# Kernel tuning notes

Measured on AMD Instinct MI355X. Metric: run time of the kernel, lower is better.

Reference implementation:

```python
import jax, jax.numpy as jnp
import numpy as np

S, B, IN, OUT = 16, 32, 1024, 1024


def setup_inputs() -> dict:
    key = jax.random.key(0)
    ks = jax.random.split(key, 7)
    return {
        "input": jax.random.normal(ks[0], (S, B, IN), dtype=jnp.float32),
        "w_mu": jax.random.normal(ks[1], (OUT, IN), dtype=jnp.float32) * 0.1 - 3.0,
        "w_std_eta": jax.random.uniform(ks[2], (OUT, IN), dtype=jnp.float32, minval=-4.0, maxval=-2.0),
        "b_mu": jax.random.normal(ks[3], (OUT,), dtype=jnp.float32) * 0.03,
        "b_std_eta": jax.random.uniform(ks[4], (OUT,), dtype=jnp.float32, minval=-0.03, maxval=0.03),
        "eps_w": jax.random.normal(ks[5], (B, OUT, IN), dtype=jnp.float32),
        "eps_b": jax.random.normal(ks[6], (B, OUT), dtype=jnp.float32),
    }


def _kl_to_std_normal(mu, std):
    # KL( N(mu, std) || N(0, 1) ) elementwise, summed
    return jnp.sum(-jnp.log(std) + 0.5 * (std * std + mu * mu) - 0.5)


def reference(input, w_mu, w_std_eta, b_mu, b_std_eta, eps_w, eps_b):
    std_w = 1e-06 + jax.nn.softplus(w_std_eta)          # [OUT, IN]
    std_b = 1e-06 + jax.nn.softplus(b_std_eta)          # [OUT]
    # per-batch-element reparameterized positive weights: [B, OUT, IN]
    w = jnp.exp(w_mu[None, :, :] + std_w[None, :, :] * eps_w)
    b = b_mu[None, :] + std_b[None, :] * eps_b          # [B, OUT]
    # batched linear: for each b-index i: input[:, i, :] @ w[i].T + b[i]
    out = jnp.einsum('sbi,boi->sbo', input, w) + b[None, :, :]  # [S, B, OUT]
    kl_w = _kl_to_std_normal(w_mu, std_w)
    kl_b = _kl_to_std_normal(b_mu, std_b)
    return (out, kl_w, kl_b)
```

## Files before the change

### kernel.cpp

```cpp
#include <hip/hip_runtime.h>


constexpr int S_ = 16, B_ = 32, IN_ = 1024, OUT_ = 1024;

typedef __bf16 bf16x8 __attribute__((ext_vector_type(8)));
typedef float  f32x4  __attribute__((ext_vector_type(4)));

__device__ __forceinline__ float softplus_f(float x) {
    float e = __expf(-fabsf(x));
    return fmaxf(x, 0.0f) + __logf(1.0f + e);
}

__device__ __forceinline__ unsigned bf16_hi(float x) {
    return (__float_as_uint(x) + 0x8000u) & 0xffff0000u;
}

__global__ __launch_bounds__(256) void bpl_pre2(
    const float* __restrict__ input,
    const float* __restrict__ w_mu, const float* __restrict__ w_eta,
    unsigned* __restrict__ tbl,
    __bf16* __restrict__ a_ws,
    float* __restrict__ klw_part)
{
    const int tid = threadIdx.x;

    if (blockIdx.x >= 1024) {
        const int b = blockIdx.x - 1024;
        #pragma unroll
        for (int j = 0; j < 8; ++j) {
            const int c  = tid + j * 256;
            const int k0 = ((c >> 6) << 5) | (((c >> 4) & 3) << 3);
            const int s  = c & 15;
            const float* src = input + ((size_t)s * B_ + b) * IN_ + k0;
            const float4 x0 = *reinterpret_cast<const float4*>(src);
            const float4 x1 = *reinterpret_cast<const float4*>(src + 4);
            bf16x8 v;
            v[0] = (__bf16)x0.x; v[1] = (__bf16)x0.y; v[2] = (__bf16)x0.z; v[3] = (__bf16)x0.w;
            v[4] = (__bf16)x1.x; v[5] = (__bf16)x1.y; v[6] = (__bf16)x1.z; v[7] = (__bf16)x1.w;
            *reinterpret_cast<bf16x8*>(&a_ws[(size_t)b * 16384 + (size_t)c * 8]) = v;
        }
        return;
    }

    __shared__ float red[4];
    const int wid  = tid >> 6;
    const int lane = tid & 63;

    const size_t base = (size_t)blockIdx.x * IN_ + tid * 4;
    const float4 mu = *reinterpret_cast<const float4*>(&w_mu[base]);
    const float4 et = *reinterpret_cast<const float4*>(&w_eta[base]);
    const float m[4] = {mu.x, mu.y, mu.z, mu.w};
    const float e[4] = {et.x, et.y, et.z, et.w};

    uint4 pk;
    unsigned* pku = &pk.x;
    float local = 0.0f;
    #pragma unroll
    for (int j = 0; j < 4; ++j) {
        const float sp  = __logf(1.0f + __expf(e[j])) + 1e-6f;
        const float spl = sp * 1.44269504f;
        const float emu = __expf(m[j]);
        pku[j] = bf16_hi(emu) | (bf16_hi(spl) >> 16);
        local += -__logf(sp) + 0.5f * fmaf(sp, sp, m[j] * m[j]) - 0.5f;
    }
    *reinterpret_cast<uint4*>(&tbl[base]) = pk;

    #pragma unroll
    for (int off = 32; off > 0; off >>= 1) local += __shfl_xor(local, off, 64);
    if (lane == 0) red[wid] = local;
    __syncthreads();
    if (tid == 0) klw_part[blockIdx.x] = red[0] + red[1] + red[2] + red[3];
}

__global__ __launch_bounds__(256, 4) void bpl_fused(
    const unsigned* __restrict__ tbl,
    const __bf16* __restrict__ a_ws,
    const float* __restrict__ eps_w,
    const float* __restrict__ b_mu,
    const float* __restrict__ b_eta,
    const float* __restrict__ eps_b,
    const float* __restrict__ klw_part,
    float* __restrict__ out,
    float* __restrict__ kl)
{
    const int blk = blockIdx.x;
    const int tid = threadIdx.x;

    if (blk == 2048) {
        __shared__ float kred[8];
        const int wid  = tid >> 6;
        const int lane = tid & 63;
        float lw = klw_part[tid] + klw_part[tid + 256]
                 + klw_part[tid + 512] + klw_part[tid + 768];
        float lb = 0.0f;
        #pragma unroll
        for (int h = 0; h < 4; ++h) {
            const int o = tid + h * 256;
            const float sd = softplus_f(b_eta[o]) + 1e-6f;
            const float mm = b_mu[o];
            lb += -__logf(sd) + 0.5f * fmaf(sd, sd, mm * mm) - 0.5f;
        }
        #pragma unroll
        for (int off = 32; off > 0; off >>= 1) {
            lw += __shfl_xor(lw, off, 64);
            lb += __shfl_xor(lb, off, 64);
        }
        if (lane == 0) { kred[wid] = lw; kred[4 + wid] = lb; }
        __syncthreads();
        if (tid == 0) {
            kl[0] = kred[0] + kred[1] + kred[2] + kred[3];
            kl[1] = kred[4] + kred[5] + kred[6] + kred[7];
        }
        return;
    }

    __shared__ __align__(16) float red[4 * 64 * 4];

    const int xcd = blk & 7;
    const int r_  = blk >> 3;
    const int b   = r_ & 31;
    const int ot  = r_ >> 5;
    const int o_base = xcd * 128 + ot * 16;

    const int kq   = tid >> 6;
    const int lane = tid & 63;
    const int on   = lane & 15;
    const int kg0  = lane >> 4;
    const int o_row = o_base + on;

    const int kbase = kq * 256 + kg0 * 8;
    const unsigned* __restrict__ tp = tbl + (size_t)o_row * IN_ + kbase;
    const float* __restrict__ ep = eps_w + ((size_t)b * OUT_ + o_row) * IN_ + kbase;
    const __bf16* __restrict__ ap = a_ws + (size_t)b * 16384 + (size_t)kq * 4096 + lane * 8;

    f32x4 acc = {0.0f, 0.0f, 0.0f, 0.0f};

    uint4  tb0[4], tb1[4];
    float4 ev0[4], ev1[4];
    bf16x8 av[4];

#define BPL_LD(T) do {                                                                    \
        ev0[(T) & 3] = *reinterpret_cast<const float4*>(ep + (T) * 32);                   \
        ev1[(T) & 3] = *reinterpret_cast<const float4*>(ep + (T) * 32 + 4);               \
        tb0[(T) & 3] = *reinterpret_cast<const uint4*>(tp + (T) * 32);                    \
        tb1[(T) & 3] = *reinterpret_cast<const uint4*>(tp + (T) * 32 + 4);                \
        av[(T) & 3]  = *reinterpret_cast<const bf16x8*>(ap + (T) * 512); } while (0)

    BPL_LD(0); BPL_LD(1); BPL_LD(2); BPL_LD(3);

    #pragma unroll
    for (int t = 0; t < 8; ++t) {
        const uint4  u0 = tb0[t & 3], u1 = tb1[t & 3];
        const float4 e0 = ev0[t & 3], e1 = ev1[t & 3];
        const bf16x8 af = av[t & 3];

        const unsigned uu[8] = {u0.x, u0.y, u0.z, u0.w, u1.x, u1.y, u1.z, u1.w};
        const float    ee[8] = {e0.x, e0.y, e0.z, e0.w, e1.x, e1.y, e1.z, e1.w};

        bf16x8 bfrag;
        #pragma unroll
        for (int q = 0; q < 8; ++q) {
            const float emu = __uint_as_float(uu[q] & 0xffff0000u);
            const float spl = __uint_as_float(uu[q] << 16);
            bfrag[q] = (__bf16)(emu * exp2f(spl * ee[q]));
        }

        if (t < 4) BPL_LD(t + 4);

        acc = __builtin_amdgcn_mfma_f32_16x16x32_bf16(af, bfrag, acc, 0, 0, 0);
    }
#undef BPL_LD

    *reinterpret_cast<f32x4*>(&red[(kq * 64 + lane) * 4]) = acc;
    __syncthreads();

    {
        const int s  = tid >> 4;
        const int ol = tid & 15;
        const int srcLane = ((s >> 2) << 4) | ol;
        const int rr = s & 3;
        float v = red[(0 * 64 + srcLane) * 4 + rr] + red[(1 * 64 + srcLane) * 4 + rr]
                + red[(2 * 64 + srcLane) * 4 + rr] + red[(3 * 64 + srcLane) * 4 + rr];
        const int oo = o_base + ol;
        const float bias = fmaf(softplus_f(b_eta[oo]) + 1e-6f,
                                eps_b[(size_t)b * OUT_ + oo], b_mu[oo]);
        out[((size_t)s * B_ + b) * OUT_ + oo] = v + bias;
    }
}

__global__ __launch_bounds__(256) void bpl_pre_fb(
    const float* __restrict__ w_mu, const float* __restrict__ w_eta,
    const float* __restrict__ b_mu, const float* __restrict__ b_eta,
    float* __restrict__ kl)
{
    __shared__ float red[4];
    const int tid  = threadIdx.x;
    const int wid  = tid >> 6;
    const int lane = tid & 63;

    const size_t base = (size_t)blockIdx.x * IN_ + tid * 4;
    const float4 mu = *reinterpret_cast<const float4*>(&w_mu[base]);
    const float4 et = *reinterpret_cast<const float4*>(&w_eta[base]);
    const float m[4] = {mu.x, mu.y, mu.z, mu.w};
    const float e[4] = {et.x, et.y, et.z, et.w};

    float local = 0.0f;
    #pragma unroll
    for (int j = 0; j < 4; ++j) {
        const float sp = __logf(1.0f + __expf(e[j])) + 1e-6f;
        local += -__logf(sp) + 0.5f * fmaf(sp, sp, m[j] * m[j]) - 0.5f;
    }
    #pragma unroll
    for (int off = 32; off > 0; off >>= 1) local += __shfl_xor(local, off, 64);
    if (lane == 0) red[wid] = local;
    __syncthreads();
    if (tid == 0) atomicAdd(&kl[0], red[0] + red[1] + red[2] + red[3]);

    if (blockIdx.x != 0) return;
    float lb = 0.0f;
    #pragma unroll
    for (int j = 0; j < 4; ++j) {
        const int idx = tid * 4 + j;
        const float sd = softplus_f(b_eta[idx]) + 1e-6f;
        const float mm = b_mu[idx];
        lb += -__logf(sd) + 0.5f * fmaf(sd, sd, mm * mm) - 0.5f;
    }
    #pragma unroll
    for (int off = 32; off > 0; off >>= 1) lb += __shfl_xor(lb, off, 64);
    __syncthreads();
    if (lane == 0) red[wid] = lb;
    __syncthreads();
    if (tid == 0) atomicAdd(&kl[1], red[0] + red[1] + red[2] + red[3]);
}

__global__ __launch_bounds__(256, 4) void bpl_mfma_fb(
    const float* __restrict__ input, const float* __restrict__ w_mu,
    const float* __restrict__ w_eta, const float* __restrict__ b_mu,
    const float* __restrict__ b_eta, const float* __restrict__ eps_w,
    const float* __restrict__ eps_b, float* __restrict__ out)
{
    __shared__ __align__(16) __bf16 alds[16384];

    const int blk = blockIdx.x;
    const int xcd = blk & 7;
    const int r_  = blk >> 3;
    const int b   = r_ & 31;
    const int oh  = r_ >> 5;
    const int o_base = (xcd * 2 + oh) * 64;

    const int tid  = threadIdx.x;
    const int wid  = tid >> 6;
    const int lane = tid & 63;

    #pragma unroll
    for (int j = 0; j < 8; ++j) {
        const int c   = tid + j * 256;
        const int s   = c & 15;
        const int kgg = ((c >> 6) << 2) | ((c >> 4) & 3);
        const float* src = input + ((size_t)s * B_ + b) * IN_ + kgg * 8;
        const float4 x0 = *reinterpret_cast<const float4*>(src);
        const float4 x1 = *reinterpret_cast<const float4*>(src + 4);
        bf16x8 v;
        v[0] = (__bf16)x0.x; v[1] = (__bf16)x0.y; v[2] = (__bf16)x0.z; v[3] = (__bf16)x0.w;
        v[4] = (__bf16)x1.x; v[5] = (__bf16)x1.y; v[6] = (__bf16)x1.z; v[7] = (__bf16)x1.w;
        *reinterpret_cast<bf16x8*>(&alds[c * 8]) = v;
    }
    __syncthreads();

    const int on    = lane & 15;
    const int kg0   = lane >> 4;
    const int o_row = o_base + wid * 16 + on;

    const float* __restrict__ mu_p = w_mu  + (size_t)o_row * IN_ + kg0 * 8;
    const float* __restrict__ et_p = w_eta + (size_t)o_row * IN_ + kg0 * 8;
    const float* __restrict__ ep_p = eps_w + ((size_t)b * OUT_ + o_row) * IN_ + kg0 * 8;
    const __bf16* __restrict__ a_p = alds + lane * 8;

    f32x4 acc = {0.0f, 0.0f, 0.0f, 0.0f};
    #pragma unroll
    for (int kt = 0; kt < 32; ++kt) {
        const int i_ = kt * 32;
        const float4 m0 = *reinterpret_cast<const float4*>(mu_p + i_);
        const float4 m1 = *reinterpret_cast<const float4*>(mu_p + i_ + 4);
        const float4 s0 = *reinterpret_cast<const float4*>(et_p + i_);
        const float4 s1 = *reinterpret_cast<const float4*>(et_p + i_ + 4);
        const float4 e0 = *reinterpret_cast<const float4*>(ep_p + i_);
        const float4 e1 = *reinterpret_cast<const float4*>(ep_p + i_ + 4);
        const float mm[8] = {m0.x, m0.y, m0.z, m0.w, m1.x, m1.y, m1.z, m1.w};
        const float ss[8] = {s0.x, s0.y, s0.z, s0.w, s1.x, s1.y, s1.z, s1.w};
        const float ee[8] = {e0.x, e0.y, e0.z, e0.w, e1.x, e1.y, e1.z, e1.w};
        bf16x8 bfrag;
        #pragma unroll
        for (int q = 0; q < 8; ++q) {
            const float sp_ = __logf(1.0f + __expf(ss[q])) + 1e-6f;
            bfrag[q] = (__bf16)__expf(fmaf(sp_, ee[q], mm[q]));
        }
        const bf16x8 afrag = *reinterpret_cast<const bf16x8*>(a_p + kt * 512);
        acc = __builtin_amdgcn_mfma_f32_16x16x32_bf16(afrag, bfrag, acc, 0, 0, 0);
    }

    const float bias = fmaf(softplus_f(b_eta[o_row]) + 1e-6f,
                            eps_b[(size_t)b * OUT_ + o_row], b_mu[o_row]);
    #pragma unroll
    for (int rr = 0; rr < 4; ++rr) {
        const int s = kg0 * 4 + rr;
        out[((size_t)s * B_ + b) * OUT_ + o_row] = acc[rr] + bias;
    }
}

extern "C" void kernel_launch(void* const* d_in, const int* in_sizes, int n_in,
                              void* d_out, int out_size, void* d_ws, size_t ws_size,
                              hipStream_t stream)
{
    const float* input = (const float*)d_in[0];
    const float* w_mu  = (const float*)d_in[1];
    const float* w_eta = (const float*)d_in[2];
    const float* b_mu  = (const float*)d_in[3];
    const float* b_eta = (const float*)d_in[4];
    const float* eps_w = (const float*)d_in[5];
    const float* eps_b = (const float*)d_in[6];

    float* out = (float*)d_out;
    float* kl  = out + (size_t)S_ * B_ * OUT_;

    const size_t TBL_OFF = 0;
    const size_t A_OFF   = (size_t)4 * 1024 * 1024;
    const size_t KLP_OFF = (size_t)5 * 1024 * 1024;
    const size_t NEED    = KLP_OFF + 4096;

    if (ws_size >= NEED) {
        unsigned* tbl  = (unsigned*)((char*)d_ws + TBL_OFF);
        __bf16*   a_ws = (__bf16*)((char*)d_ws + A_OFF);
        float*    klp  = (float*)((char*)d_ws + KLP_OFF);

        bpl_pre2<<<1056, 256, 0, stream>>>(input, w_mu, w_eta, tbl, a_ws, klp);
        bpl_fused<<<2049, 256, 0, stream>>>(tbl, a_ws, eps_w, b_mu, b_eta, eps_b,
                                            klp, out, kl);
    } else {
        hipMemsetAsync(kl, 0, 2 * sizeof(float), stream);
        bpl_pre_fb<<<1024, 256, 0, stream>>>(w_mu, w_eta, b_mu, b_eta, kl);
        bpl_mfma_fb<<<512, 256, 0, stream>>>(input, w_mu, w_eta, b_mu, b_eta,
                                             eps_w, eps_b, out);
    }
}
```

Measured before the change: 43.91 us.

## Stage eps_w through swizzled LDS and pre-permute weight table into fragment order

The fused kernel now uses 512 threads with 8 k-quarters. Each wave loads eps_w rows with fully coalesced float2 reads, stages them in XOR-swizzled shared memory, then reads them back in MFMA fragment order. The precompute kernel writes the packed exp(mu)/softplus table directly in fragment-major layout, so the fused kernel's table loads are contiguous per lane. The goal is to fix strided global access to eps_w and the table, at the cost of 64KB of LDS per block, an extra barrier, and lost software pipelining of loads against compute.

```diff
diff --git a/kernel.cpp b/kernel.cpp
--- a/kernel.cpp
+++ b/kernel.cpp
@@ -18,7 +18,7 @@
 __global__ __launch_bounds__(256) void bpl_pre2(
     const float* __restrict__ input,
     const float* __restrict__ w_mu, const float* __restrict__ w_eta,
-    unsigned* __restrict__ tbl,
+    unsigned* __restrict__ tbl_f,
     __bf16* __restrict__ a_ws,
     float* __restrict__ klw_part)
 {
@@ -45,25 +45,31 @@
     __shared__ float red[4];
     const int wid  = tid >> 6;
     const int lane = tid & 63;
-
-    const size_t base = (size_t)blockIdx.x * IN_ + tid * 4;
+    const int o    = blockIdx.x;
+    const int ot   = o >> 4;
+    const int on   = o & 15;
+
+    const size_t base = (size_t)o * IN_ + tid * 4;
     const float4 mu = *reinterpret_cast<const float4*>(&w_mu[base]);
     const float4 et = *reinterpret_cast<const float4*>(&w_eta[base]);
     const float m[4] = {mu.x, mu.y, mu.z, mu.w};
     const float e[4] = {et.x, et.y, et.z, et.w};
 
-    uint4 pk;
-    unsigned* pku = &pk.x;
     float local = 0.0f;
     #pragma unroll
     for (int j = 0; j < 4; ++j) {
+        const int   i   = tid * 4 + j;
         const float sp  = __logf(1.0f + __expf(e[j])) + 1e-6f;
         const float spl = sp * 1.44269504f;
         const float emu = __expf(m[j]);
-        pku[j] = bf16_hi(emu) | (bf16_hi(spl) >> 16);
+        const unsigned pk = bf16_hi(emu) | (bf16_hi(spl) >> 16);
+        const int kt  = i >> 5;
+        const int kg0 = (i >> 3) & 3;
+        const int jj  = i & 7;
+        const int ln  = kg0 * 16 + on;
+        tbl_f[(((size_t)ot * 32 + kt) * 64 + ln) * 8 + jj] = pk;
         local += -__logf(sp) + 0.5f * fmaf(sp, sp, m[j] * m[j]) - 0.5f;
     }
-    *reinterpret_cast<uint4*>(&tbl[base]) = pk;
 
     #pragma unroll
     for (int off = 32; off > 0; off >>= 1) local += __shfl_xor(local, off, 64);
@@ -72,8 +78,8 @@
     if (tid == 0) klw_part[blockIdx.x] = red[0] + red[1] + red[2] + red[3];
 }
 
-__global__ __launch_bounds__(256, 4) void bpl_fused(
-    const unsigned* __restrict__ tbl,
+__global__ __launch_bounds__(512, 4) void bpl_fused(
+    const unsigned* __restrict__ tbl_f,
     const __bf16* __restrict__ a_ws,
     const float* __restrict__ eps_w,
     const float* __restrict__ b_mu,
@@ -87,75 +93,91 @@
     const int tid = threadIdx.x;
 
     if (blk == 2048) {
-        __shared__ float kred[8];
+        __shared__ float kred[16];
         const int wid  = tid >> 6;
         const int lane = tid & 63;
-        float lw = klw_part[tid] + klw_part[tid + 256]
-                 + klw_part[tid + 512] + klw_part[tid + 768];
+        float lw = klw_part[tid & 1023] * 0.0f;
+        lw = ((tid < 512) ? klw_part[tid] + klw_part[tid + 512] : 0.0f);
         float lb = 0.0f;
-        #pragma unroll
-        for (int h = 0; h < 4; ++h) {
-            const int o = tid + h * 256;
-            const float sd = softplus_f(b_eta[o]) + 1e-6f;
-            const float mm = b_mu[o];
-            lb += -__logf(sd) + 0.5f * fmaf(sd, sd, mm * mm) - 0.5f;
+        {
+            const int o = tid;
+            const float sd0 = softplus_f(b_eta[o]) + 1e-6f;
+            const float m0  = b_mu[o];
+            const float sd1 = softplus_f(b_eta[o + 512]) + 1e-6f;
+            const float m1  = b_mu[o + 512];
+            lb = (-__logf(sd0) + 0.5f * fmaf(sd0, sd0, m0 * m0) - 0.5f)
+               + (-__logf(sd1) + 0.5f * fmaf(sd1, sd1, m1 * m1) - 0.5f);
         }
         #pragma unroll
         for (int off = 32; off > 0; off >>= 1) {
             lw += __shfl_xor(lw, off, 64);
             lb += __shfl_xor(lb, off, 64);
         }
-        if (lane == 0) { kred[wid] = lw; kred[4 + wid] = lb; }
+        if (lane == 0) { kred[wid] = lw; kred[8 + wid] = lb; }
         __syncthreads();
         if (tid == 0) {
-            kl[0] = kred[0] + kred[1] + kred[2] + kred[3];
-            kl[1] = kred[4] + kred[5] + kred[6] + kred[7];
+            float tw = 0.0f, tb = 0.0f;
+            #pragma unroll
+            for (int k = 0; k < 8; ++k) { tw += kred[k]; tb += kred[8 + k]; }
+            kl[0] = tw; kl[1] = tb;
         }
         return;
     }
 
-    __shared__ __align__(16) float red[4 * 64 * 4];
+    __shared__ __align__(16) float smem[16384];
 
     const int xcd = blk & 7;
     const int r_  = blk >> 3;
     const int b   = r_ & 31;
-    const int ot  = r_ >> 5;
-    const int o_base = xcd * 128 + ot * 16;
+    const int otl = r_ >> 5;
+    const int o_base = xcd * 128 + otl * 16;
+    const int ot_g   = o_base >> 4;
 
     const int kq   = tid >> 6;
     const int lane = tid & 63;
     const int on   = lane & 15;
     const int kg0  = lane >> 4;
-    const int o_row = o_base + on;
-
-    const int kbase = kq * 256 + kg0 * 8;
-    const unsigned* __restrict__ tp = tbl + (size_t)o_row * IN_ + kbase;
-    const float* __restrict__ ep = eps_w + ((size_t)b * OUT_ + o_row) * IN_ + kbase;
-    const __bf16* __restrict__ ap = a_ws + (size_t)b * 16384 + (size_t)kq * 4096 + lane * 8;
+
+    const float* eps_base = eps_w + ((size_t)(b * 1024 + o_base)) * 1024 + kq * 128;
+    float2 ev[16];
+    #pragma unroll
+    for (int r = 0; r < 16; ++r)
+        ev[r] = *reinterpret_cast<const float2*>(eps_base + (size_t)r * 1024 + lane * 2);
+
+    const unsigned* tf = tbl_f + (((size_t)ot_g * 32 + kq * 4) * 64 + lane) * 8;
+    uint4 t0[4], t1[4];
+    #pragma unroll
+    for (int t = 0; t < 4; ++t) {
+        t0[t] = *reinterpret_cast<const uint4*>(tf + t * 512);
+        t1[t] = *reinterpret_cast<const uint4*>(tf + t * 512 + 4);
+    }
+
+    const __bf16* ap = a_ws + (size_t)b * 16384 + (size_t)(kq * 4) * 512 + lane * 8;
+    bf16x8 av[4];
+    #pragma unroll
+    for (int t = 0; t < 4; ++t)
+        av[t] = *reinterpret_cast<const bf16x8*>(ap + t * 512);
+
+    char* wbase = (char*)(smem + kq * 2048);
+    #pragma unroll
+    for (int r = 0; r < 16; ++r) {
+        const int byte = (lane * 8) ^ ((r & 7) << 4);
+        *reinterpret_cast<float2*>(wbase + r * 512 + byte) = ev[r];
+    }
+    __syncthreads();
 
     f32x4 acc = {0.0f, 0.0f, 0.0f, 0.0f};
-
-    uint4  tb0[4], tb1[4];
-    float4 ev0[4], ev1[4];
-    bf16x8 av[4];
-
-#define BPL_LD(T) do {                                                                    \
-        ev0[(T) & 3] = *reinterpret_cast<const float4*>(ep + (T) * 32);                   \
-        ev1[(T) & 3] = *reinterpret_cast<const float4*>(ep + (T) * 32 + 4);               \
-        tb0[(T) & 3] = *reinterpret_cast<const uint4*>(tp + (T) * 32);                    \
-        tb1[(T) & 3] = *reinterpret_cast<const uint4*>(tp + (T) * 32 + 4);                \
-        av[(T) & 3]  = *reinterpret_cast<const bf16x8*>(ap + (T) * 512); } while (0)
-
-    BPL_LD(0); BPL_LD(1); BPL_LD(2); BPL_LD(3);
-
-    #pragma unroll
-    for (int t = 0; t < 8; ++t) {
-        const uint4  u0 = tb0[t & 3], u1 = tb1[t & 3];
-        const float4 e0 = ev0[t & 3], e1 = ev1[t & 3];
-        const bf16x8 af = av[t & 3];
-
-        const unsigned uu[8] = {u0.x, u0.y, u0.z, u0.w, u1.x, u1.y, u1.z, u1.w};
-        const float    ee[8] = {e0.x, e0.y, e0.z, e0.w, e1.x, e1.y, e1.z, e1.w};
+    const int sw = (on & 7) << 4;
+    #pragma unroll
+    for (int t = 0; t < 4; ++t) {
+        const f32x4 e0 = *reinterpret_cast<const f32x4*>(
+            wbase + on * 512 + (((t * 128 + kg0 * 32)) ^ sw));
+        const f32x4 e1 = *reinterpret_cast<const f32x4*>(
+            wbase + on * 512 + (((t * 128 + kg0 * 32 + 16)) ^ sw));
+
+        const unsigned uu[8] = {t0[t].x, t0[t].y, t0[t].z, t0[t].w,
+                                t1[t].x, t1[t].y, t1[t].z, t1[t].w};
+        const float    ee[8] = {e0[0], e0[1], e0[2], e0[3], e1[0], e1[1], e1[2], e1[3]};
 
         bf16x8 bfrag;
         #pragma unroll
@@ -164,23 +186,22 @@
             const float spl = __uint_as_float(uu[q] << 16);
             bfrag[q] = (__bf16)(emu * exp2f(spl * ee[q]));
         }
-
-        if (t < 4) BPL_LD(t + 4);
-
-        acc = __builtin_amdgcn_mfma_f32_16x16x32_bf16(af, bfrag, acc, 0, 0, 0);
-    }
-#undef BPL_LD
-
-    *reinterpret_cast<f32x4*>(&red[(kq * 64 + lane) * 4]) = acc;
-    __syncthreads();
-
-    {
+        acc = __builtin_amdgcn_mfma_f32_16x16x32_bf16(av[t], bfrag, acc, 0, 0, 0);
+    }
+
+    __syncthreads();
+    *reinterpret_cast<f32x4*>(&smem[(kq * 64 + lane) * 4]) = acc;
+    __syncthreads();
+
+    if (tid < 256) {
         const int s  = tid >> 4;
         const int ol = tid & 15;
         const int srcLane = ((s >> 2) << 4) | ol;
         const int rr = s & 3;
-        float v = red[(0 * 64 + srcLane) * 4 + rr] + red[(1 * 64 + srcLane) * 4 + rr]
-                + red[(2 * 64 + srcLane) * 4 + rr] + red[(3 * 64 + srcLane) * 4 + rr];
+        float v = 0.0f;
+        #pragma unroll
+        for (int k8 = 0; k8 < 8; ++k8)
+            v += smem[((k8 * 64 + srcLane) * 4) + rr];
         const int oo = o_base + ol;
         const float bias = fmaf(softplus_f(b_eta[oo]) + 1e-6f,
                                 eps_b[(size_t)b * OUT_ + oo], b_mu[oo]);
@@ -334,7 +355,7 @@
         float*    klp  = (float*)((char*)d_ws + KLP_OFF);
 
         bpl_pre2<<<1056, 256, 0, stream>>>(input, w_mu, w_eta, tbl, a_ws, klp);
-        bpl_fused<<<2049, 256, 0, stream>>>(tbl, a_ws, eps_w, b_mu, b_eta, eps_b,
+        bpl_fused<<<2049, 512, 0, stream>>>(tbl, a_ws, eps_w, b_mu, b_eta, eps_b,
                                             klp, out, kl);
     } else {
         hipMemsetAsync(kl, 0, 2 * sizeof(float), stream);
```

New measurement: 37.69 us. -14.2%, faster.
